# Optimization experiments

Measured on AMD Instinct MI355X. Metric: run time of the kernel, lower is better.

The kernel has to match this reference:

```python
import jax, jax.numpy as jnp
import numpy as np

W0_SIREN = 30.0  # omega_0 used in sine activations

HID = [64, 64, 256, 256, 256]
IN_DIM = 65   # 64 feat channels + 1 time channel
OUT_DIM = 64


def _siren_params(key):
    dims = [IN_DIM] + HID + [OUT_DIM]
    params = []
    for i in range(len(dims) - 1):
        fan_in, fan_out = dims[i], dims[i + 1]
        key, kw, kb = jax.random.split(key, 3)
        if i == 0:
            bound = 1.0 / fan_in
        else:
            bound = np.sqrt(6.0 / fan_in) / W0_SIREN
        W = jax.random.uniform(kw, (fan_out, fan_in), jnp.float32, -bound, bound)
        b = jax.random.uniform(kb, (fan_out,), jnp.float32, -bound, bound)
        params.append((W, b))
    return params


def setup_inputs() -> dict:
    key = jax.random.key(0)
    k_feat, k_t, k_p = jax.random.split(key, 3)
    feat = jax.random.normal(k_feat, (2, 64, 192, 320), jnp.float32)
    times = jax.random.uniform(k_t, (3,), jnp.float32)
    params = _siren_params(k_p)
    inp = {"feat": feat, "times": times}
    for i, (W, b) in enumerate(params):
        inp[f"w{i}"] = W
        inp[f"b{i}"] = b
    return inp


def _gather_full_grid(feat):
    """Nearest grid_sample (align_corners=False) at pixel-center coords over the full grid.
    Returns [B, H*W, C]."""
    B, C, H, W = feat.shape
    # make_coord pixel centers in [-1, 1]
    ys = -1.0 + (2.0 * jnp.arange(H, dtype=jnp.float32) + 1.0) / H
    xs = -1.0 + (2.0 * jnp.arange(W, dtype=jnp.float32) + 1.0) / W
    gy, gx = jnp.meshgrid(ys, xs, indexing="ij")          # [H, W] each
    gy, gx = gy.reshape(-1), gx.reshape(-1)               # [qs]
    # grid_sample nearest, align_corners=False unnormalization
    iy = jnp.clip(jnp.round(((gy + 1.0) * H - 1.0) / 2.0).astype(jnp.int32), 0, H - 1)
    ix = jnp.clip(jnp.round(((gx + 1.0) * W - 1.0) / 2.0).astype(jnp.int32), 0, W - 1)
    q = feat[:, :, iy, ix]                                # [B, C, qs] gather
    return jnp.transpose(q, (0, 2, 1))                    # [B, qs, C]


def _siren_mlp(x, ws, bs):
    h = x
    n = len(ws)
    for i in range(n - 1):
        h = jnp.sin(W0_SIREN * (h @ ws[i].T + bs[i]))
    return h @ ws[n - 1].T + bs[n - 1]                    # outermost linear


def reference(feat, times, w0, b0, w1, b1, w2, b2, w3, b3, w4, b4, w5, b5):
    ws = [w0, w1, w2, w3, w4, w5]
    bs = [b0, b1, b2, b3, b4, b5]
    B, C, H, W = feat.shape
    qs = H * W
    q_feat = _gather_full_grid(feat)                      # [B, qs, 64]
    preds = []
    for c in range(3):  # Training==True branch: 3 time stamps
        t = times[c]
        pe = jnp.full((B, qs, 1), 1.0, feat.dtype) * t    # time channel
        enc = jnp.concatenate([q_feat, pe], axis=-1)      # [B, qs, 65]
        out = _siren_mlp(enc.reshape(B * qs, IN_DIM), ws, bs)  # [B*qs, 64]
        # F.fold with kernel_size=1 == reshape back to spatial map
        pred = out.reshape(B, qs, OUT_DIM).transpose(0, 2, 1).reshape(B, OUT_DIM, H, W)
        preds.append(pred)
    return jnp.stack(preds, axis=0)                       # [3, B, 64, H, W]
```

## Files before the change

### kernel.cpp

```cpp
#include <hip/hip_runtime.h>
#include <hip/hip_bf16.h>

typedef __bf16 bf16_t;
typedef bf16_t bf16x8 __attribute__((ext_vector_type(8)));
typedef float f32x4 __attribute__((ext_vector_type(4)));
typedef unsigned short u16;
typedef unsigned int u32;

static constexpr int kHW = 192 * 320;
static constexpr float kC = 4.77464829275686f;

__device__ __forceinline__ u16 f2bf(float f) {
  u32 u = __float_as_uint(f);
  return (u16)((u + 0x7FFFu + ((u >> 16) & 1u)) >> 16);
}

__device__ __forceinline__ u32 pack2(float a, float b) {
  __hip_bfloat162 h = __float22bfloat162_rn(make_float2(a, b));
  union { __hip_bfloat162 h2; u32 u; } cv;
  cv.h2 = h;
  return cv.u;
}

static constexpr int OFF_W0 = 0;
static constexpr int OFF_W1 = 4096;
static constexpr int OFF_W2 = 8192;
static constexpr int OFF_W3 = 24576;
static constexpr int OFF_W4 = 90112;
static constexpr int OFF_W5 = 155648;
static constexpr int W_TOTAL = 172032;
static constexpr int B_TOTAL = 1024;

__global__ void convert_weights(const float* __restrict__ w0, const float* __restrict__ w1,
                                const float* __restrict__ w2, const float* __restrict__ w3,
                                const float* __restrict__ w4, const float* __restrict__ w5,
                                const float* __restrict__ b0, const float* __restrict__ b1,
                                const float* __restrict__ b2, const float* __restrict__ b3,
                                const float* __restrict__ b4, const float* __restrict__ b5,
                                u16* __restrict__ wb, float* __restrict__ bws) {
  int i = blockIdx.x * 256 + threadIdx.x;
  if (i < W_TOTAL) {
    float v, s = kC;
    if (i < OFF_W1)      { int o = i >> 6, k = i & 63; v = w0[o * 65 + k]; }
    else if (i < OFF_W2) { v = w1[i - OFF_W1]; }
    else if (i < OFF_W3) { v = w2[i - OFF_W2]; }
    else if (i < OFF_W4) { v = w3[i - OFF_W3]; }
    else if (i < OFF_W5) { v = w4[i - OFF_W4]; }
    else                 { v = w5[i - OFF_W5]; s = 1.0f; }
    wb[i] = f2bf(v * s);
  } else {
    int j = i - W_TOTAL;
    float v;
    if (j < 64)       v = kC * b0[j];
    else if (j < 128) v = kC * w0[(j - 64) * 65 + 64];
    else if (j < 192) v = kC * b1[j - 128];
    else if (j < 448) v = kC * b2[j - 192];
    else if (j < 704) v = kC * b3[j - 448];
    else if (j < 960) v = kC * b4[j - 704];
    else              v = b5[j - 960];
    bws[j] = v;
  }
}

template<int K, int NOT, int NPT, bool LAST>
__device__ __forceinline__ void layer_fn(const u16* __restrict__ wb, const float* bias,
                                         const u16* act_in, u16* act_out,
                                         float* __restrict__ out_base,
                                         int o_tile0, int pt0, int lane) {
  constexpr int KT = K / 32;
  const int l15  = lane & 15;
  const int quad = lane >> 4;
  const int sw   = l15 & 7;

  bf16x8 wf[NOT][KT];
  f32x4  bv[NOT];
#pragma unroll
  for (int ot = 0; ot < NOT; ++ot) {
    const int o = (o_tile0 + ot) * 16 + l15;
#pragma unroll
    for (int ks = 0; ks < KT; ++ks)
      wf[ot][ks] = *reinterpret_cast<const bf16x8*>(wb + o * K + ks * 32 + quad * 8);
    bv[ot] = *reinterpret_cast<const f32x4*>(bias + (o_tile0 + ot) * 16 + quad * 4);
  }

#pragma unroll 1
  for (int ip = 0; ip < NPT; ++ip) {
    const int p = (pt0 + ip) * 16 + l15;
    bf16x8 af[KT];
#pragma unroll
    for (int ks = 0; ks < KT; ++ks)
      af[ks] = *reinterpret_cast<const bf16x8*>(act_in + p * 256 + (((ks * 4 + quad) ^ sw) * 8));

#pragma unroll
    for (int ot = 0; ot < NOT; ++ot) {
      f32x4 acc = bv[ot];
#pragma unroll
      for (int ks = 0; ks < KT; ++ks)
        acc = __builtin_amdgcn_mfma_f32_16x16x32_bf16(wf[ot][ks], af[ks], acc, 0, 0, 0);

      if constexpr (LAST) {
        const int o = (o_tile0 + ot) * 16 + quad * 4;
        float* dst = out_base + (size_t)o * kHW + p;
#pragma unroll
        for (int r = 0; r < 4; ++r) dst[(size_t)r * kHW] = acc[r];
      } else {
        float s0 = __builtin_amdgcn_sinf(__builtin_amdgcn_fractf(acc[0]));
        float s1 = __builtin_amdgcn_sinf(__builtin_amdgcn_fractf(acc[1]));
        float s2 = __builtin_amdgcn_sinf(__builtin_amdgcn_fractf(acc[2]));
        float s3 = __builtin_amdgcn_sinf(__builtin_amdgcn_fractf(acc[3]));
        uint2 v;
        v.x = pack2(s0, s1);
        v.y = pack2(s2, s3);
        const int g = (o_tile0 + ot) * 2 + (quad >> 1);
        *reinterpret_cast<uint2*>(act_out + p * 256 + ((g ^ sw) * 8) + (quad & 1) * 4) = v;
      }
    }
  }
}

__global__ void __launch_bounds__(512, 4)
siren_main(const float* __restrict__ feat, const float* __restrict__ times,
           const u16* __restrict__ wb, const float* __restrict__ bws,
           float* __restrict__ out) {
  __shared__ __align__(16) u16 actA[64 * 256];
  __shared__ __align__(16) u16 actB[64 * 256];
  __shared__ __align__(16) float bias_lds[960];

  const int tid = threadIdx.x;
  const int bid = blockIdx.x;
  const int c   = bid / 1920;
  const int pb  = bid % 1920;
  const int p0  = pb * 64;
  const int bq  = p0 / kHW;
  const int hw0 = p0 % kHW;
  const float t = times[c];

  if (tid < 64) bias_lds[tid] = bws[tid] + t * bws[64 + tid];
  for (int i = tid; i < 896; i += 512) bias_lds[64 + i] = bws[128 + i];

  {
    const float* fbase = feat + (size_t)bq * 64 * kHW + hw0;
    const int p = tid & 63;
    const int g = tid >> 6;
    float v[8];
#pragma unroll
    for (int j = 0; j < 8; ++j) v[j] = fbase[(size_t)(g * 8 + j) * kHW + p];
    uint4 pk;
    pk.x = pack2(v[0], v[1]);
    pk.y = pack2(v[2], v[3]);
    pk.z = pack2(v[4], v[5]);
    pk.w = pack2(v[6], v[7]);
    *reinterpret_cast<uint4*>(actA + p * 256 + ((g ^ (p & 7)) * 8)) = pk;
  }
  __syncthreads();

  const int wave = tid >> 6;
  const int lane = tid & 63;
  float* out_base = out + (size_t)(c * 2 + bq) * 64 * kHW + hw0;

  const int ot64  = wave & 3;
  const int pt64  = (wave >> 2) * 2;
  const int ot256 = wave * 2;

  layer_fn<64, 1, 2, false>(wb + OFF_W0, bias_lds + 0,   actA, actB, nullptr, ot64, pt64, lane);
  __syncthreads();
  layer_fn<64, 1, 2, false>(wb + OFF_W1, bias_lds + 64,  actB, actA, nullptr, ot64, pt64, lane);
  __syncthreads();
  layer_fn<64, 2, 4, false>(wb + OFF_W2, bias_lds + 128, actA, actB, nullptr, ot256, 0, lane);
  __syncthreads();
  layer_fn<256, 2, 4, false>(wb + OFF_W3, bias_lds + 384, actB, actA, nullptr, ot256, 0, lane);
  __syncthreads();
  layer_fn<256, 2, 4, false>(wb + OFF_W4, bias_lds + 640, actA, actB, nullptr, ot256, 0, lane);
  __syncthreads();
  layer_fn<256, 1, 2, true >(wb + OFF_W5, bias_lds + 896, actB, nullptr, out_base, ot64, pt64, lane);
}

extern "C" void kernel_launch(void* const* d_in, const int* in_sizes, int n_in,
                              void* d_out, int out_size, void* d_ws, size_t ws_size,
                              hipStream_t stream) {
  const float* feat  = (const float*)d_in[0];
  const float* times = (const float*)d_in[1];
  const float* w0 = (const float*)d_in[2];
  const float* b0 = (const float*)d_in[3];
  const float* w1 = (const float*)d_in[4];
  const float* b1 = (const float*)d_in[5];
  const float* w2 = (const float*)d_in[6];
  const float* b2 = (const float*)d_in[7];
  const float* w3 = (const float*)d_in[8];
  const float* b3 = (const float*)d_in[9];
  const float* w4 = (const float*)d_in[10];
  const float* b4 = (const float*)d_in[11];
  const float* w5 = (const float*)d_in[12];
  const float* b5 = (const float*)d_in[13];
  u16*   wb  = (u16*)d_ws;
  float* bws = (float*)((char*)d_ws + (size_t)W_TOTAL * 2);
  float* out = (float*)d_out;

  convert_weights<<<(W_TOTAL + B_TOTAL) / 256, 256, 0, stream>>>(
      w0, w1, w2, w3, w4, w5, b0, b1, b2, b3, b4, b5, wb, bws);
  siren_main<<<5760, 512, 0, stream>>>(feat, times, wb, bws, out);
}
```

Measured before the change: 403.1 us.

## Restructure SIREN kernel with 256-thread blocks, register-blocked layers, and pre-packed features

Each block now runs 4 waves instead of 8, and every wave owns four 16-row output tiles of the 256-wide layers. Activation fragments are double-buffered in registers so the next point tile loads while the MFMAs run. A separate convert_feat kernel packs the feature map to bf16 once, so the three time steps copy ready-made tiles instead of gathering strided fp32 data three times. The time-dependent bias is folded in registers and the LDS bias staging is gone. In exchange, per-thread register pressure rises, there is an extra kernel launch, and a fallback path is used when the workspace is too small.

Result: no change. 408.7 us (+1.4%).

```diff
diff --git a/kernel.cpp b/kernel.cpp
--- a/kernel.cpp
+++ b/kernel.cpp
@@ -30,6 +30,8 @@
 static constexpr int OFF_W5 = 155648;
 static constexpr int W_TOTAL = 172032;
 static constexpr int B_TOTAL = 1024;
+static constexpr size_t FEAT_BYTE_OFF = 348160;
+static constexpr size_t WS_NEED = FEAT_BYTE_OFF + (size_t)1920 * 8192;
 
 __global__ void convert_weights(const float* __restrict__ w0, const float* __restrict__ w1,
                                 const float* __restrict__ w2, const float* __restrict__ w3,
@@ -62,117 +64,212 @@
   }
 }
 
-template<int K, int NOT, int NPT, bool LAST>
-__device__ __forceinline__ void layer_fn(const u16* __restrict__ wb, const float* bias,
-                                         const u16* act_in, u16* act_out,
-                                         float* __restrict__ out_base,
-                                         int o_tile0, int pt0, int lane) {
-  constexpr int KT = K / 32;
-  const int l15  = lane & 15;
-  const int quad = lane >> 4;
-  const int sw   = l15 & 7;
-
-  bf16x8 wf[NOT][KT];
-  f32x4  bv[NOT];
-#pragma unroll
-  for (int ot = 0; ot < NOT; ++ot) {
-    const int o = (o_tile0 + ot) * 16 + l15;
-#pragma unroll
-    for (int ks = 0; ks < KT; ++ks)
-      wf[ot][ks] = *reinterpret_cast<const bf16x8*>(wb + o * K + ks * 32 + quad * 8);
-    bv[ot] = *reinterpret_cast<const f32x4*>(bias + (o_tile0 + ot) * 16 + quad * 4);
-  }
-
-#pragma unroll 1
-  for (int ip = 0; ip < NPT; ++ip) {
-    const int p = (pt0 + ip) * 16 + l15;
-    bf16x8 af[KT];
-#pragma unroll
-    for (int ks = 0; ks < KT; ++ks)
-      af[ks] = *reinterpret_cast<const bf16x8*>(act_in + p * 256 + (((ks * 4 + quad) ^ sw) * 8));
-
-#pragma unroll
-    for (int ot = 0; ot < NOT; ++ot) {
-      f32x4 acc = bv[ot];
-#pragma unroll
-      for (int ks = 0; ks < KT; ++ks)
-        acc = __builtin_amdgcn_mfma_f32_16x16x32_bf16(wf[ot][ks], af[ks], acc, 0, 0, 0);
-
-      if constexpr (LAST) {
-        const int o = (o_tile0 + ot) * 16 + quad * 4;
-        float* dst = out_base + (size_t)o * kHW + p;
-#pragma unroll
-        for (int r = 0; r < 4; ++r) dst[(size_t)r * kHW] = acc[r];
-      } else {
-        float s0 = __builtin_amdgcn_sinf(__builtin_amdgcn_fractf(acc[0]));
-        float s1 = __builtin_amdgcn_sinf(__builtin_amdgcn_fractf(acc[1]));
-        float s2 = __builtin_amdgcn_sinf(__builtin_amdgcn_fractf(acc[2]));
-        float s3 = __builtin_amdgcn_sinf(__builtin_amdgcn_fractf(acc[3]));
-        uint2 v;
-        v.x = pack2(s0, s1);
-        v.y = pack2(s2, s3);
-        const int g = (o_tile0 + ot) * 2 + (quad >> 1);
-        *reinterpret_cast<uint2*>(act_out + p * 256 + ((g ^ sw) * 8) + (quad & 1) * 4) = v;
-      }
-    }
-  }
-}
-
-__global__ void __launch_bounds__(512, 4)
-siren_main(const float* __restrict__ feat, const float* __restrict__ times,
-           const u16* __restrict__ wb, const float* __restrict__ bws,
-           float* __restrict__ out) {
-  __shared__ __align__(16) u16 actA[64 * 256];
-  __shared__ __align__(16) u16 actB[64 * 256];
-  __shared__ __align__(16) float bias_lds[960];
-
+__global__ void convert_feat(const float* __restrict__ feat, u16* __restrict__ featT) {
+  const int chunk = blockIdx.x;
+  const int bq  = chunk / 960;
+  const int hw0 = (chunk % 960) * 64;
   const int tid = threadIdx.x;
-  const int bid = blockIdx.x;
-  const int c   = bid / 1920;
-  const int pb  = bid % 1920;
-  const int p0  = pb * 64;
-  const int bq  = p0 / kHW;
-  const int hw0 = p0 % kHW;
-  const float t = times[c];
-
-  if (tid < 64) bias_lds[tid] = bws[tid] + t * bws[64 + tid];
-  for (int i = tid; i < 896; i += 512) bias_lds[64 + i] = bws[128 + i];
-
-  {
-    const float* fbase = feat + (size_t)bq * 64 * kHW + hw0;
-    const int p = tid & 63;
-    const int g = tid >> 6;
+  const int p   = tid & 63;
+  const int gg  = tid >> 6;
+  const float* fbase = feat + (size_t)bq * 64 * kHW + hw0 + p;
+  u16* img = featT + (size_t)chunk * 4096;
+#pragma unroll
+  for (int j = 0; j < 2; ++j) {
+    const int g = gg * 2 + j;
     float v[8];
 #pragma unroll
-    for (int j = 0; j < 8; ++j) v[j] = fbase[(size_t)(g * 8 + j) * kHW + p];
+    for (int e = 0; e < 8; ++e) v[e] = fbase[(size_t)(g * 8 + e) * kHW];
     uint4 pk;
     pk.x = pack2(v[0], v[1]);
     pk.y = pack2(v[2], v[3]);
     pk.z = pack2(v[4], v[5]);
     pk.w = pack2(v[6], v[7]);
-    *reinterpret_cast<uint4*>(actA + p * 256 + ((g ^ (p & 7)) * 8)) = pk;
-  }
-  __syncthreads();
-
-  const int wave = tid >> 6;
-  const int lane = tid & 63;
+    *reinterpret_cast<uint4*>(img + p * 64 + ((g ^ (p & 7)) * 8)) = pk;
+  }
+}
+
+template<int RSO>
+__device__ __forceinline__ void epilogue_sin(f32x4 acc, u16* outb, int p, int g,
+                                             int quad, int sw) {
+  float s0 = __builtin_amdgcn_sinf(__builtin_amdgcn_fractf(acc[0]));
+  float s1 = __builtin_amdgcn_sinf(__builtin_amdgcn_fractf(acc[1]));
+  float s2 = __builtin_amdgcn_sinf(__builtin_amdgcn_fractf(acc[2]));
+  float s3 = __builtin_amdgcn_sinf(__builtin_amdgcn_fractf(acc[3]));
+  uint2 v;
+  v.x = pack2(s0, s1);
+  v.y = pack2(s2, s3);
+  *reinterpret_cast<uint2*>(outb + p * RSO + ((g ^ sw) * 8) + (quad & 1) * 4) = v;
+}
+
+template<int NOT, int RSI, int RSO, bool TB>
+__device__ __forceinline__ void layer_small(const u16* __restrict__ wb,
+                                            const float* __restrict__ bg,
+                                            const float* __restrict__ bgt, float t,
+                                            const u16* in, u16* outb, int wave, int lane) {
+  const int l15 = lane & 15, quad = lane >> 4, sw = l15 & 7;
+  bf16x8 wf[NOT][2];
+  f32x4  bv[NOT];
+#pragma unroll
+  for (int ot = 0; ot < NOT; ++ot) {
+    const int got = wave * NOT + ot;
+#pragma unroll
+    for (int ks = 0; ks < 2; ++ks)
+      wf[ot][ks] = *reinterpret_cast<const bf16x8*>(wb + (got * 16 + l15) * 64 + ks * 32 + quad * 8);
+    f32x4 b0 = *reinterpret_cast<const f32x4*>(bg + got * 16 + quad * 4);
+    if constexpr (TB) {
+      f32x4 b1 = *reinterpret_cast<const f32x4*>(bgt + got * 16 + quad * 4);
+#pragma unroll
+      for (int r = 0; r < 4; ++r) bv[ot][r] = b0[r] + t * b1[r];
+    } else {
+      bv[ot] = b0;
+    }
+  }
+  bf16x8 af[4][2];
+#pragma unroll
+  for (int pt = 0; pt < 4; ++pt)
+#pragma unroll
+    for (int ks = 0; ks < 2; ++ks)
+      af[pt][ks] = *reinterpret_cast<const bf16x8*>(
+          in + (pt * 16 + l15) * RSI + (((ks * 4 + quad) ^ sw) * 8));
+#pragma unroll
+  for (int pt = 0; pt < 4; ++pt) {
+    const int p = pt * 16 + l15;
+#pragma unroll
+    for (int ot = 0; ot < NOT; ++ot) {
+      f32x4 acc = bv[ot];
+      acc = __builtin_amdgcn_mfma_f32_16x16x32_bf16(wf[ot][0], af[pt][0], acc, 0, 0, 0);
+      acc = __builtin_amdgcn_mfma_f32_16x16x32_bf16(wf[ot][1], af[pt][1], acc, 0, 0, 0);
+      epilogue_sin<RSO>(acc, outb, p, (wave * NOT + ot) * 2 + (quad >> 1), quad, sw);
+    }
+  }
+}
+
+template<int NOT, int PPAR, int RSO, bool LAST>
+__device__ __forceinline__ void layer_big(const u16* __restrict__ wb,
+                                          const float* __restrict__ bg,
+                                          const u16* in, u16* outb,
+                                          float* __restrict__ outg, int wave, int lane) {
+  const int l15 = lane & 15, quad = lane >> 4, sw = l15 & 7;
+  bf16x8 wf[NOT][8];
+#pragma unroll
+  for (int ks = 0; ks < 8; ++ks)
+#pragma unroll
+    for (int ot = 0; ot < NOT; ++ot)
+      wf[ot][ks] = *reinterpret_cast<const bf16x8*>(
+          wb + ((wave * NOT + ot) * 16 + l15) * 256 + ks * 32 + quad * 8);
+  f32x4 bv[NOT];
+#pragma unroll
+  for (int ot = 0; ot < NOT; ++ot)
+    bv[ot] = *reinterpret_cast<const f32x4*>(bg + (wave * NOT + ot) * 16 + quad * 4);
+
+  constexpr int G = 4 / PPAR;
+  bf16x8 af[2][PPAR][8];
+#pragma unroll
+  for (int pp = 0; pp < PPAR; ++pp)
+#pragma unroll
+    for (int ks = 0; ks < 8; ++ks)
+      af[0][pp][ks] = *reinterpret_cast<const bf16x8*>(
+          in + (pp * 16 + l15) * 256 + (((ks * 4 + quad) ^ sw) * 8));
+
+#pragma unroll
+  for (int g = 0; g < G; ++g) {
+    if (g + 1 < G) {
+#pragma unroll
+      for (int pp = 0; pp < PPAR; ++pp)
+#pragma unroll
+        for (int ks = 0; ks < 8; ++ks)
+          af[(g + 1) & 1][pp][ks] = *reinterpret_cast<const bf16x8*>(
+              in + (((g + 1) * PPAR + pp) * 16 + l15) * 256 + (((ks * 4 + quad) ^ sw) * 8));
+    }
+    f32x4 acc[PPAR][NOT];
+#pragma unroll
+    for (int pp = 0; pp < PPAR; ++pp)
+#pragma unroll
+      for (int ot = 0; ot < NOT; ++ot) acc[pp][ot] = bv[ot];
+#pragma unroll
+    for (int ks = 0; ks < 8; ++ks)
+#pragma unroll
+      for (int pp = 0; pp < PPAR; ++pp)
+#pragma unroll
+        for (int ot = 0; ot < NOT; ++ot)
+          acc[pp][ot] = __builtin_amdgcn_mfma_f32_16x16x32_bf16(
+              wf[ot][ks], af[g & 1][pp][ks], acc[pp][ot], 0, 0, 0);
+#pragma unroll
+    for (int pp = 0; pp < PPAR; ++pp) {
+      const int p = (g * PPAR + pp) * 16 + l15;
+#pragma unroll
+      for (int ot = 0; ot < NOT; ++ot) {
+        if constexpr (LAST) {
+          const int o = (wave * NOT + ot) * 16 + quad * 4;
+          float* dst = outg + (size_t)o * kHW + p;
+#pragma unroll
+          for (int r = 0; r < 4; ++r) dst[(size_t)r * kHW] = acc[pp][ot][r];
+        } else {
+          epilogue_sin<RSO>(acc[pp][ot], outb, p,
+                            (wave * NOT + ot) * 2 + (quad >> 1), quad, sw);
+        }
+      }
+    }
+  }
+}
+
+template<bool PRE>
+__global__ void __launch_bounds__(256, 2)
+siren_main(const float* __restrict__ feat, const float* __restrict__ times,
+           const u16* __restrict__ wb, const float* __restrict__ bws,
+           const u16* __restrict__ featT, float* __restrict__ out) {
+  __shared__ __align__(16) u16 A32[64 * 256];
+  __shared__ __align__(16) u16 B32[64 * 256];
+  u16* X = B32;
+  u16* Y = B32 + 4096;
+
+  const int tid   = threadIdx.x;
+  const int bid   = blockIdx.x;
+  const int c     = bid / 1920;
+  const int chunk = bid % 1920;
+  const int bq    = chunk / 960;
+  const int hw0   = (chunk % 960) * 64;
+  const float t   = times[c];
+  const int wave  = tid >> 6;
+  const int lane  = tid & 63;
+
+  if constexpr (PRE) {
+    const uint4* src = reinterpret_cast<const uint4*>(featT + (size_t)chunk * 4096);
+    uint4* dst = reinterpret_cast<uint4*>(X);
+    dst[tid]       = src[tid];
+    dst[tid + 256] = src[tid + 256];
+  } else {
+    const int p  = tid & 63;
+    const int gg = tid >> 6;
+    const float* fbase = feat + (size_t)bq * 64 * kHW + hw0 + p;
+#pragma unroll
+    for (int j = 0; j < 2; ++j) {
+      const int g = gg * 2 + j;
+      float v[8];
+#pragma unroll
+      for (int e = 0; e < 8; ++e) v[e] = fbase[(size_t)(g * 8 + e) * kHW];
+      uint4 pk;
+      pk.x = pack2(v[0], v[1]);
+      pk.y = pack2(v[2], v[3]);
+      pk.z = pack2(v[4], v[5]);
+      pk.w = pack2(v[6], v[7]);
+      *reinterpret_cast<uint4*>(X + p * 64 + ((g ^ (p & 7)) * 8)) = pk;
+    }
+  }
+  __syncthreads();
+
+  layer_small<1, 64, 64, true >(wb + OFF_W0, bws + 0,   bws + 64, t, X, Y, wave, lane);
+  __syncthreads();
+  layer_small<1, 64, 64, false>(wb + OFF_W1, bws + 128, nullptr, 0.f, Y, X, wave, lane);
+  __syncthreads();
+  layer_small<4, 64, 256, false>(wb + OFF_W2, bws + 192, nullptr, 0.f, X, A32, wave, lane);
+  __syncthreads();
+  layer_big<4, 1, 256, false>(wb + OFF_W3, bws + 448, A32, B32, nullptr, wave, lane);
+  __syncthreads();
+  layer_big<4, 1, 256, false>(wb + OFF_W4, bws + 704, B32, A32, nullptr, wave, lane);
+  __syncthreads();
   float* out_base = out + (size_t)(c * 2 + bq) * 64 * kHW + hw0;
-
-  const int ot64  = wave & 3;
-  const int pt64  = (wave >> 2) * 2;
-  const int ot256 = wave * 2;
-
-  layer_fn<64, 1, 2, false>(wb + OFF_W0, bias_lds + 0,   actA, actB, nullptr, ot64, pt64, lane);
-  __syncthreads();
-  layer_fn<64, 1, 2, false>(wb + OFF_W1, bias_lds + 64,  actB, actA, nullptr, ot64, pt64, lane);
-  __syncthreads();
-  layer_fn<64, 2, 4, false>(wb + OFF_W2, bias_lds + 128, actA, actB, nullptr, ot256, 0, lane);
-  __syncthreads();
-  layer_fn<256, 2, 4, false>(wb + OFF_W3, bias_lds + 384, actB, actA, nullptr, ot256, 0, lane);
-  __syncthreads();
-  layer_fn<256, 2, 4, false>(wb + OFF_W4, bias_lds + 640, actA, actB, nullptr, ot256, 0, lane);
-  __syncthreads();
-  layer_fn<256, 1, 2, true >(wb + OFF_W5, bias_lds + 896, actB, nullptr, out_base, ot64, pt64, lane);
+  layer_big<1, 2, 256, true>(wb + OFF_W5, bws + 960, A32, nullptr, out_base, wave, lane);
 }
 
 extern "C" void kernel_launch(void* const* d_in, const int* in_sizes, int n_in,
@@ -198,5 +295,12 @@
 
   convert_weights<<<(W_TOTAL + B_TOTAL) / 256, 256, 0, stream>>>(
       w0, w1, w2, w3, w4, w5, b0, b1, b2, b3, b4, b5, wb, bws);
-  siren_main<<<5760, 512, 0, stream>>>(feat, times, wb, bws, out);
-}
+
+  if (ws_size >= WS_NEED) {
+    u16* featT = (u16*)((char*)d_ws + FEAT_BYTE_OFF);
+    convert_feat<<<1920, 256, 0, stream>>>(feat, featT);
+    siren_main<true><<<5760, 256, 0, stream>>>(feat, times, wb, bws, featT, out);
+  } else {
+    siren_main<false><<<5760, 256, 0, stream>>>(feat, times, wb, bws, wb, out);
+  }
+}
```
